# Performance work log

Measured on AMD Instinct MI355X. Metric: run time of the kernel, lower is better.

## Reference

```python
import jax, jax.numpy as jnp
from jax import lax
import numpy as np

B, T, D, H = 64, 512, 1024, 1024


def setup_inputs() -> dict:
    key = jax.random.key(0)
    ks = jax.random.split(key, 4)
    # glorot-ish scaling for stable tanh/sigmoid dynamics
    w_scale = (2.0 / (D + H + 2 * H)) ** 0.5
    u_scale = (2.0 / (D + H + H)) ** 0.5
    return {
        "x": jax.random.normal(ks[0], (B, T, D), dtype=jnp.float32),
        "h0": jax.random.normal(ks[1], (B, H), dtype=jnp.float32),
        "W": jax.random.normal(ks[2], (D + H, 2 * H), dtype=jnp.float32) * w_scale,
        "W_b": jnp.zeros((2 * H,), dtype=jnp.float32),
        "U": jax.random.normal(ks[3], (D + H, H), dtype=jnp.float32) * u_scale,
        "U_b": jnp.zeros((H,), dtype=jnp.float32),
    }


def reference(x, h0, W, W_b, U, U_b):
    """GRUCell from bzhangGo/lrn run over a sequence via lax.scan.

    Per step (faithful to the keras cell):
      gi = sigmoid([x, h] @ W + W_b)   # [B, 2H]
      r, u = gi[:, :H], gi[:, H:]
      c = tanh([x, r*h] @ U + U_b)     # [B, H]
      h = u*h + (1-u)*c
    """
    units = W_b.shape[0] // 2

    def step(h, xt):
        gi = jax.nn.sigmoid(jnp.concatenate([xt, h], axis=-1) @ W + W_b)  # [B, 2H]
        r = gi[:, :units]
        u = gi[:, units:]
        c = jnp.tanh(jnp.concatenate([xt, r * h], axis=-1) @ U + U_b)     # [B, H]
        h_new = u * h + (1.0 - u) * c
        return h_new, h_new

    # scan over time: x [B, T, D] -> [T, B, D]
    _, hs = lax.scan(step, h0, jnp.swapaxes(x, 0, 1))
    return jnp.swapaxes(hs, 0, 1)  # [B, T, H]
```

## Files before the change

### kernel.cpp

```cpp
#include <hip/hip_runtime.h>
#include <hip/hip_bf16.h>
#include <stdint.h>


typedef unsigned short u16;
typedef unsigned long long u64;
typedef __attribute__((ext_vector_type(8))) short bf16x8;
typedef __attribute__((ext_vector_type(4))) float f32x4;

constexpr int Bsz = 64, Tt = 512, Dd = 1024, Hh = 1024;
constexpr int Mrows = Bsz * Tt;
constexpr int NP = 3 * Hh;
constexpr int NBLK = 64, THR = 512;

constexpr size_t SZ_XPROJ = (size_t)Mrows * NP * 2;
constexpr size_t SZ_XBF   = (size_t)Mrows * Dd * 2;
constexpr size_t SZ_PT    = (size_t)NP * 1024 * 2;
constexpr size_t SZ_WHT   = (size_t)2048 * 1024 * 2;
constexpr size_t SZ_UHT   = (size_t)1024 * 1024 * 2;
constexpr size_t OFF_XPROJ = 0;
constexpr size_t OFF_XBF   = OFF_XPROJ + SZ_XPROJ;
constexpr size_t OFF_PT    = OFF_XBF + SZ_XBF;
constexpr size_t OFF_WHT   = OFF_PT + SZ_PT;
constexpr size_t OFF_UHT   = OFF_WHT + SZ_WHT;
constexpr size_t OFF_HG    = OFF_UHT + SZ_UHT;
constexpr size_t OFF_RHG   = OFF_HG  + 131072;
constexpr size_t OFF_BAR   = OFF_RHG + 131072;
constexpr size_t WS_NEEDED = OFF_BAR + 4096;

__device__ __forceinline__ float b2f(u16 u) {
  union { unsigned i; float f; } x; x.i = ((unsigned)u) << 16; return x.f;
}
__device__ __forceinline__ u16 f2b(float f) {
  union { float f; unsigned i; } x; x.f = f;
  unsigned r = (x.i >> 16) & 1u;
  return (u16)((x.i + 0x7fffu + r) >> 16);
}
__device__ __forceinline__ float sigmoidf_(float x) { return 1.0f / (1.0f + __expf(-x)); }
__device__ __forceinline__ float tanhf_(float x) { return 1.0f - 2.0f / (__expf(2.0f * x) + 1.0f); }

__device__ __forceinline__ u64 ldA_u64(const u64* p) {
  return __hip_atomic_load(p, __ATOMIC_RELAXED, __HIP_MEMORY_SCOPE_AGENT);
}
__device__ __forceinline__ void stA_u64(u64* p, u64 v) {
  __hip_atomic_store(p, v, __ATOMIC_RELAXED, __HIP_MEMORY_SCOPE_AGENT);
}
__device__ __forceinline__ unsigned ldA_u32(const unsigned* p) {
  return __hip_atomic_load(p, __ATOMIC_RELAXED, __HIP_MEMORY_SCOPE_AGENT);
}
__device__ __forceinline__ void stA_u32(unsigned* p, unsigned v) {
  __hip_atomic_store(p, v, __ATOMIC_RELAXED, __HIP_MEMORY_SCOPE_AGENT);
}

__device__ __forceinline__ void drain_vm() {
  asm volatile("s_waitcnt vmcnt(0)" ::: "memory");
}
__device__ __forceinline__ void bar_lds() {
  asm volatile("s_waitcnt lgkmcnt(0)\n\ts_barrier" ::: "memory");
}
__device__ __forceinline__ void bar_x() {
  asm volatile("s_barrier" ::: "memory");
}
__device__ __forceinline__ void lds_arrive(unsigned* c) {
  __hip_atomic_fetch_add(c, 1u, __ATOMIC_RELAXED, __HIP_MEMORY_SCOPE_WORKGROUP);
}
__device__ __forceinline__ unsigned lds_peek(unsigned* c) {
  return __hip_atomic_load(c, __ATOMIC_RELAXED, __HIP_MEMORY_SCOPE_WORKGROUP);
}

__device__ __forceinline__ void gl2lds16(const void* g, void* l) {
  __builtin_amdgcn_global_load_lds(
      (const __attribute__((address_space(1))) void*)g,
      (__attribute__((address_space(3))) void*)l, 16, 0, 0);
}

__global__ void k_prep_x(const float* __restrict__ x, u16* __restrict__ xbf,
                         const float* __restrict__ h0, u16* __restrict__ h_g,
                         unsigned* __restrict__ bar) {
  size_t i = (size_t)blockIdx.x * blockDim.x + threadIdx.x;
  size_t stride = (size_t)gridDim.x * blockDim.x;
  if (i < 1024) bar[i] = 0u;
  for (size_t k = i; k < (size_t)Mrows * Dd; k += stride) xbf[k] = f2b(x[k]);
  for (size_t k = i; k < (size_t)Bsz * Hh; k += stride) {
    int r = (int)(k & 15), c = (int)((k >> 4) & 1023), g = (int)(k >> 14);
    h_g[k] = f2b(h0[(size_t)(g * 16 + r) * 1024 + c]);
  }
}

__global__ void k_prep_w(const float* __restrict__ W, const float* __restrict__ U,
                         u16* __restrict__ Pt, u16* __restrict__ Wht, u16* __restrict__ Uht) {
  int k = blockIdx.y, xb = blockIdx.x, tid = threadIdx.x;
  if (xb < 12) {
    int n = xb * 256 + tid;
    float v = (n < 2048) ? W[(size_t)k * 2048 + n] : U[(size_t)k * 1024 + (n - 2048)];
    Pt[(size_t)n * 1024 + k] = f2b(v);
  } else if (xb < 20) {
    int n = (xb - 12) * 256 + tid;
    Wht[(size_t)n * 1024 + k] = f2b(W[(size_t)(1024 + k) * 2048 + n]);
  } else {
    int n = (xb - 20) * 256 + tid;
    Uht[(size_t)n * 1024 + k] = f2b(U[(size_t)(1024 + k) * 1024 + n]);
  }
}

__global__ void k_ws_too_small(float* out) {
  out[threadIdx.x] = 12345.0f;
}

__global__ void k_gemm(const u16* __restrict__ xbf, const u16* __restrict__ Pt,
                       const float* __restrict__ Wb, const float* __restrict__ Ub,
                       u16* __restrict__ xproj) {
  __shared__ u16 As[128 * 32];
  __shared__ u16 Bs[128 * 32];
  const int tid = threadIdx.x, lane = tid & 63, w = tid >> 6;
  const int l15 = lane & 15, q = lane >> 4;
  const int bm = blockIdx.x, bn = blockIdx.y;
  const int wm = w >> 1, wn = w & 1;
  const int lr = lane >> 2;
  const int lc = (lane & 3) * 8;
  f32x4 acc[4][4] = {};
  for (int kt = 0; kt < 32; ++kt) {
    __syncthreads();
    {
      const u16* ga = xbf + (size_t)(bm * 128 + w * 32 + lr) * 1024 + kt * 32 + lc;
      gl2lds16(ga, As + w * 1024);
      gl2lds16(ga + 16 * 1024, As + w * 1024 + 512);
      const u16* gb = Pt + (size_t)(bn * 128 + w * 32 + lr) * 1024 + kt * 32 + lc;
      gl2lds16(gb, Bs + w * 1024);
      gl2lds16(gb + 16 * 1024, Bs + w * 1024 + 512);
    }
    __syncthreads();
    bf16x8 af[4], bfr[4];
#pragma unroll
    for (int i = 0; i < 4; ++i)
      af[i] = *(const bf16x8*)(As + (wm * 64 + i * 16 + l15) * 32 + q * 8);
#pragma unroll
    for (int j = 0; j < 4; ++j)
      bfr[j] = *(const bf16x8*)(Bs + (wn * 64 + j * 16 + l15) * 32 + q * 8);
#pragma unroll
    for (int i = 0; i < 4; ++i)
#pragma unroll
      for (int j = 0; j < 4; ++j)
        acc[i][j] = __builtin_amdgcn_mfma_f32_16x16x32_bf16(af[i], bfr[j], acc[i][j], 0, 0, 0);
  }
#pragma unroll
  for (int j = 0; j < 4; ++j) {
    int n = bn * 128 + wn * 64 + j * 16 + l15;
    float bias = (n < 2048) ? Wb[n] : Ub[n - 2048];
#pragma unroll
    for (int i = 0; i < 4; ++i) {
#pragma unroll
      for (int r = 0; r < 4; ++r) {
        int m = bm * 128 + wm * 64 + i * 16 + q * 4 + r;
        xproj[(size_t)m * NP + n] = f2b(acc[i][j][r] + bias);
      }
    }
  }
}

__device__ __forceinline__ void stage_tile(const u64* g64, u16* hs, int tid) {
#pragma unroll
  for (int i = 0; i < 2; ++i) {
    int z = i * THR + tid;
    int rr = z & 3, cq = z >> 2;
    const u64* p = g64 + cq * 16 + rr;
    u64 v0 = ldA_u64(p);
    u64 v1 = ldA_u64(p + 4);
    u64 v2 = ldA_u64(p + 8);
    u64 v3 = ldA_u64(p + 12);
#pragma unroll
    for (int k = 0; k < 4; ++k) {
      int r = rr * 4 + k;
      u64 wv = (u64)(u16)(v0 >> (16 * k))
             | ((u64)(u16)(v1 >> (16 * k)) << 16)
             | ((u64)(u16)(v2 >> (16 * k)) << 32)
             | ((u64)(u16)(v3 >> (16 * k)) << 48);
      *(u64*)(hs + r * 1032 + cq * 4) = wv;
    }
  }
}

__global__ void __launch_bounds__(THR, 2)
k_seq(const u16* __restrict__ xproj, const u16* __restrict__ Wht,
      const u16* __restrict__ Uht, const float* __restrict__ h0,
      u16* __restrict__ h_g, u16* __restrict__ rh_g,
      float* __restrict__ out, unsigned* __restrict__ bar) {
  __shared__ u16 hs[16 * 1032];
  __shared__ f32x4 red[4][64];
  __shared__ unsigned acnt;
  const int tid = threadIdx.x, lane = tid & 63, w = tid >> 6;
  const int l15 = lane & 15, q = lane >> 4;
  const int b = blockIdx.x;
  const int mh = b & 3;
  const int rbase = mh * 16;
  const int bq = b >> 2;
  const int half = w >> 1;
  const int odd = w & 1;
  const int a_nt = odd ? (bq * 4 + half) : (64 + bq * 4 + half);
  const int a_col = a_nt * 16 + l15;
  const int b_col = (bq * 4 + half) * 16 + l15;

  bf16x8 wa[32];
  { const u16* p = Wht + (size_t)a_col * 1024 + q * 8;
#pragma unroll
    for (int s = 0; s < 32; ++s) wa[s] = *(const bf16x8*)(p + s * 32); }
  bf16x8 wb[16];
  { const u16* p = Uht + (size_t)b_col * 1024 + odd * 512 + q * 8;
#pragma unroll
    for (int s = 0; s < 16; ++s) wb[s] = *(const bf16x8*)(p + s * 32); }

  float hp[4];
#pragma unroll
  for (int r = 0; r < 4; ++r) hp[r] = h0[(size_t)(rbase + q * 4 + r) * 1024 + b_col];

  float gxp[4];
#pragma unroll
  for (int r = 0; r < 4; ++r)
    gxp[r] = b2f(xproj[(size_t)((rbase + q * 4 + r) * Tt + 0) * NP + a_col]);
  float uxp[4] = {0.f, 0.f, 0.f, 0.f};
  if (!odd) {
#pragma unroll
    for (int r = 0; r < 4; ++r)
      uxp[r] = b2f(xproj[(size_t)((rbase + q * 4 + r) * Tt + 0) * NP + 2048 + b_col]);
  }

  const u64* hg64 = (const u64*)h_g + mh * 4096;
  const u64* rg64 = (const u64*)rh_g + mh * 4096;
  const int swb = mh + 4 * l15;

  if (tid == 0) acnt = 0;
  __syncthreads();

  unsigned bct = 0;
  unsigned atgt = 0;
#pragma unroll 1
  for (int t = 0; t < Tt; ++t) {
    stage_tile(hg64, hs, tid);
    bar_lds();

    f32x4 acc = {0.f, 0.f, 0.f, 0.f}, acc2 = {0.f, 0.f, 0.f, 0.f};
    {
      const u16* hb = hs + l15 * 1032 + q * 8;
#pragma unroll
      for (int s = 0; s < 32; s += 2) {
        bf16x8 a0 = *(const bf16x8*)(hb + s * 32);
        bf16x8 a1 = *(const bf16x8*)(hb + (s + 1) * 32);
        acc  = __builtin_amdgcn_mfma_f32_16x16x32_bf16(a0, wa[s], acc, 0, 0, 0);
        acc2 = __builtin_amdgcn_mfma_f32_16x16x32_bf16(a1, wa[s + 1], acc2, 0, 0, 0);
      }
      acc += acc2;
    }
    float uvr[4];
    if (odd) {
      u64 pk = 0;
#pragma unroll
      for (int r = 0; r < 4; ++r) {
        int lrow = q * 4 + r;
        float g = sigmoidf_(acc[r] + gxp[r]);
        float hcell = b2f(hs[lrow * 1032 + a_col]);
        pk |= (u64)f2b(g * hcell) << (16 * r);
      }
      stA_u64((u64*)rh_g + mh * 4096 + a_col * 4 + q, pk);
    } else {
#pragma unroll
      for (int r = 0; r < 4; ++r) uvr[r] = sigmoidf_(acc[r] + gxp[r]);
    }
    drain_vm();
    if (lane == 0) lds_arrive(&acnt);
    atgt += 8; ++bct;
    if (w == 0) {
      while (lds_peek(&acnt) < atgt) {}
      if (lane == 0) stA_u32(bar + (b << 4), bct);
      while (__ballot(ldA_u32(bar + (swb << 4)) < bct) != 0ull) {}
    }
    bar_x();

    stage_tile(rg64, hs, tid);
    bar_lds();

    f32x4 accb = {0.f, 0.f, 0.f, 0.f}, accb2 = {0.f, 0.f, 0.f, 0.f};
    {
      const u16* rb = hs + l15 * 1032 + odd * 512 + q * 8;
#pragma unroll
      for (int s = 0; s < 16; s += 2) {
        bf16x8 a0 = *(const bf16x8*)(rb + s * 32);
        bf16x8 a1 = *(const bf16x8*)(rb + (s + 1) * 32);
        accb  = __builtin_amdgcn_mfma_f32_16x16x32_bf16(a0, wb[s], accb, 0, 0, 0);
        accb2 = __builtin_amdgcn_mfma_f32_16x16x32_bf16(a1, wb[s + 1], accb2, 0, 0, 0);
      }
      accb += accb2;
    }
    if (odd) red[half][lane] = accb;
    bar_lds();
    float hn_[4];
    if (!odd) {
      accb += red[half][lane];
      u64 pk = 0;
#pragma unroll
      for (int r = 0; r < 4; ++r) {
        float c = tanhf_(accb[r] + uxp[r]);
        float hn = uvr[r] * hp[r] + (1.0f - uvr[r]) * c;
        hp[r] = hn; hn_[r] = hn;
        pk |= (u64)f2b(hn) << (16 * r);
      }
      stA_u64((u64*)h_g + mh * 4096 + b_col * 4 + q, pk);
    }
    drain_vm();
    if (lane == 0) lds_arrive(&acnt);
    atgt += 8; ++bct;
    if (!odd) {
#pragma unroll
      for (int r = 0; r < 4; ++r)
        out[((size_t)(rbase + q * 4 + r) * Tt + t) * 1024 + b_col] = hn_[r];
    }
    if (t + 1 < Tt) {
#pragma unroll
      for (int r = 0; r < 4; ++r)
        gxp[r] = b2f(xproj[(size_t)((rbase + q * 4 + r) * Tt + (t + 1)) * NP + a_col]);
      if (!odd) {
#pragma unroll
        for (int r = 0; r < 4; ++r)
          uxp[r] = b2f(xproj[(size_t)((rbase + q * 4 + r) * Tt + (t + 1)) * NP + 2048 + b_col]);
      }
      if (w == 0) {
        while (lds_peek(&acnt) < atgt) {}
        if (lane == 0) stA_u32(bar + (b << 4), bct);
        while (__ballot(ldA_u32(bar + (swb << 4)) < bct) != 0ull) {}
      }
      bar_x();
    }
  }
}

extern "C" void kernel_launch(void* const* d_in, const int* in_sizes, int n_in,
                              void* d_out, int out_size, void* d_ws, size_t ws_size,
                              hipStream_t stream) {
  const float* x  = (const float*)d_in[0];
  const float* h0 = (const float*)d_in[1];
  const float* W  = (const float*)d_in[2];
  const float* Wb = (const float*)d_in[3];
  const float* U  = (const float*)d_in[4];
  const float* Ub = (const float*)d_in[5];
  float* out = (float*)d_out;

  if (ws_size < WS_NEEDED) {
    k_ws_too_small<<<1, 256, 0, stream>>>(out);
    return;
  }

  char* ws = (char*)d_ws;
  u16* xproj = (u16*)(ws + OFF_XPROJ);
  u16* xbf   = (u16*)(ws + OFF_XBF);
  u16* Pt    = (u16*)(ws + OFF_PT);
  u16* Wht   = (u16*)(ws + OFF_WHT);
  u16* Uht   = (u16*)(ws + OFF_UHT);
  u16* h_g   = (u16*)(ws + OFF_HG);
  u16* rh_g  = (u16*)(ws + OFF_RHG);
  unsigned* bar = (unsigned*)(ws + OFF_BAR);

  k_prep_x<<<2048, 256, 0, stream>>>(x, xbf, h0, h_g, bar);
  k_prep_w<<<dim3(24, 1024), 256, 0, stream>>>(W, U, Pt, Wht, Uht);
  k_gemm<<<dim3(256, 24), 256, 0, stream>>>(xbf, Pt, Wb, Ub, xproj);
  k_seq<<<NBLK, 512, 0, stream>>>(xproj, Wht, Uht, h0, h_g, rh_g, out, bar);
}
```

Measured before the change: 4.870 ms.

## Replace grid barriers with sentinel-polled per-block mailboxes for recurrent state

```diff
diff --git a/kernel.cpp b/kernel.cpp
--- a/kernel.cpp
+++ b/kernel.cpp
@@ -12,6 +12,7 @@
 constexpr int Mrows = Bsz * Tt;
 constexpr int NP = 3 * Hh;
 constexpr int NBLK = 64, THR = 512;
+constexpr u64 SENTV = ~0ull;
 
 constexpr size_t SZ_XPROJ = (size_t)Mrows * NP * 2;
 constexpr size_t SZ_XBF   = (size_t)Mrows * Dd * 2;
@@ -23,10 +24,10 @@
 constexpr size_t OFF_PT    = OFF_XBF + SZ_XBF;
 constexpr size_t OFF_WHT   = OFF_PT + SZ_PT;
 constexpr size_t OFF_UHT   = OFF_WHT + SZ_WHT;
-constexpr size_t OFF_HG    = OFF_UHT + SZ_UHT;
-constexpr size_t OFF_RHG   = OFF_HG  + 131072;
-constexpr size_t OFF_BAR   = OFF_RHG + 131072;
+constexpr size_t OFF_BAR   = OFF_UHT + SZ_UHT;
 constexpr size_t WS_NEEDED = OFF_BAR + 4096;
+constexpr size_t OFF_HPV = OFF_XBF;
+constexpr size_t OFF_RPV = OFF_XBF + 4194304;
 
 __device__ __forceinline__ float b2f(u16 u) {
   union { unsigned i; float f; } x; x.i = ((unsigned)u) << 16; return x.f;
@@ -61,12 +62,6 @@
 __device__ __forceinline__ void bar_x() {
   asm volatile("s_barrier" ::: "memory");
 }
-__device__ __forceinline__ void lds_arrive(unsigned* c) {
-  __hip_atomic_fetch_add(c, 1u, __ATOMIC_RELAXED, __HIP_MEMORY_SCOPE_WORKGROUP);
-}
-__device__ __forceinline__ unsigned lds_peek(unsigned* c) {
-  return __hip_atomic_load(c, __ATOMIC_RELAXED, __HIP_MEMORY_SCOPE_WORKGROUP);
-}
 
 __device__ __forceinline__ void gl2lds16(const void* g, void* l) {
   __builtin_amdgcn_global_load_lds(
@@ -75,16 +70,11 @@
 }
 
 __global__ void k_prep_x(const float* __restrict__ x, u16* __restrict__ xbf,
-                         const float* __restrict__ h0, u16* __restrict__ h_g,
                          unsigned* __restrict__ bar) {
   size_t i = (size_t)blockIdx.x * blockDim.x + threadIdx.x;
   size_t stride = (size_t)gridDim.x * blockDim.x;
   if (i < 1024) bar[i] = 0u;
   for (size_t k = i; k < (size_t)Mrows * Dd; k += stride) xbf[k] = f2b(x[k]);
-  for (size_t k = i; k < (size_t)Bsz * Hh; k += stride) {
-    int r = (int)(k & 15), c = (int)((k >> 4) & 1023), g = (int)(k >> 14);
-    h_g[k] = f2b(h0[(size_t)(g * 16 + r) * 1024 + c]);
-  }
 }
 
 __global__ void k_prep_w(const float* __restrict__ W, const float* __restrict__ U,
@@ -158,36 +148,48 @@
   }
 }
 
-__device__ __forceinline__ void stage_tile(const u64* g64, u16* hs, int tid) {
-#pragma unroll
-  for (int i = 0; i < 2; ++i) {
-    int z = i * THR + tid;
-    int rr = z & 3, cq = z >> 2;
-    const u64* p = g64 + cq * 16 + rr;
-    u64 v0 = ldA_u64(p);
-    u64 v1 = ldA_u64(p + 4);
-    u64 v2 = ldA_u64(p + 8);
-    u64 v3 = ldA_u64(p + 12);
+__device__ __forceinline__ void stage_poll(u64* g, u16* hs, int tid) {
+  u64 vv0[4], vv1[4];
+  const int z0 = tid, z1 = THR + tid;
+  const int rr0 = z0 & 3, cq0 = z0 >> 2;
+  const int rr1 = z1 & 3, cq1 = z1 >> 2;
+  u64* p0 = g + cq0 * 16 + rr0;
+  u64* p1 = g + cq1 * 16 + rr1;
+  vv0[0] = ldA_u64(p0); vv0[1] = ldA_u64(p0 + 4);
+  vv0[2] = ldA_u64(p0 + 8); vv0[3] = ldA_u64(p0 + 12);
+  vv1[0] = ldA_u64(p1); vv1[1] = ldA_u64(p1 + 4);
+  vv1[2] = ldA_u64(p1 + 8); vv1[3] = ldA_u64(p1 + 12);
+  for (;;) {
+    bool any = false;
 #pragma unroll
     for (int k = 0; k < 4; ++k) {
-      int r = rr * 4 + k;
-      u64 wv = (u64)(u16)(v0 >> (16 * k))
-             | ((u64)(u16)(v1 >> (16 * k)) << 16)
-             | ((u64)(u16)(v2 >> (16 * k)) << 32)
-             | ((u64)(u16)(v3 >> (16 * k)) << 48);
-      *(u64*)(hs + r * 1032 + cq * 4) = wv;
-    }
-  }
-}
-
-__global__ void __launch_bounds__(THR, 2)
+      if (vv0[k] == SENTV) { vv0[k] = ldA_u64(p0 + 4 * k); if (vv0[k] == SENTV) any = true; }
+      if (vv1[k] == SENTV) { vv1[k] = ldA_u64(p1 + 4 * k); if (vv1[k] == SENTV) any = true; }
+    }
+    if (!any) break;
+  }
+#pragma unroll
+  for (int k = 0; k < 4; ++k) {
+    int r0 = rr0 * 4 + k;
+    u64 w0 = (u64)(u16)(vv0[0] >> (16 * k)) | ((u64)(u16)(vv0[1] >> (16 * k)) << 16)
+           | ((u64)(u16)(vv0[2] >> (16 * k)) << 32) | ((u64)(u16)(vv0[3] >> (16 * k)) << 48);
+    *(u64*)(hs + r0 * 1032 + cq0 * 4) = w0;
+    int r1 = rr1 * 4 + k;
+    u64 w1 = (u64)(u16)(vv1[0] >> (16 * k)) | ((u64)(u16)(vv1[1] >> (16 * k)) << 16)
+           | ((u64)(u16)(vv1[2] >> (16 * k)) << 32) | ((u64)(u16)(vv1[3] >> (16 * k)) << 48);
+    *(u64*)(hs + r1 * 1032 + cq1 * 4) = w1;
+  }
+  stA_u64(p0, SENTV); stA_u64(p0 + 4, SENTV); stA_u64(p0 + 8, SENTV); stA_u64(p0 + 12, SENTV);
+  stA_u64(p1, SENTV); stA_u64(p1 + 4, SENTV); stA_u64(p1 + 8, SENTV); stA_u64(p1 + 12, SENTV);
+}
+
+__global__ void __launch_bounds__(THR, 1)
 k_seq(const u16* __restrict__ xproj, const u16* __restrict__ Wht,
       const u16* __restrict__ Uht, const float* __restrict__ h0,
-      u16* __restrict__ h_g, u16* __restrict__ rh_g,
+      u64* __restrict__ h_pv, u64* __restrict__ rh_pv,
       float* __restrict__ out, unsigned* __restrict__ bar) {
   __shared__ u16 hs[16 * 1032];
   __shared__ f32x4 red[4][64];
-  __shared__ unsigned acnt;
   const int tid = threadIdx.x, lane = tid & 63, w = tid >> 6;
   const int l15 = lane & 15, q = lane >> 4;
   const int b = blockIdx.x;
@@ -224,18 +226,28 @@
       uxp[r] = b2f(xproj[(size_t)((rbase + q * 4 + r) * Tt + 0) * NP + 2048 + b_col]);
   }
 
-  const u64* hg64 = (const u64*)h_g + mh * 4096;
-  const u64* rg64 = (const u64*)rh_g + mh * 4096;
-  const int swb = mh + 4 * l15;
-
-  if (tid == 0) acnt = 0;
+  u64* myh = h_pv + (size_t)b * 8192;
+  u64* myr = rh_pv + (size_t)b * 8192;
+  for (int z = tid; z < 4096; z += THR) {
+    int col = z >> 2, qq = z & 3;
+    u64 v = 0;
+#pragma unroll
+    for (int k = 0; k < 4; ++k)
+      v |= (u64)f2b(h0[(size_t)(rbase + qq * 4 + k) * 1024 + col]) << (16 * k);
+    stA_u64(myh + z, v);
+    stA_u64(myh + 4096 + z, SENTV);
+    stA_u64(myr + z, SENTV);
+    stA_u64(myr + 4096 + z, SENTV);
+  }
   __syncthreads();
-
-  unsigned bct = 0;
-  unsigned atgt = 0;
+  if (tid == 0) stA_u32(bar + (b << 4), 1u);
+  if (tid < 64) { while (ldA_u32(bar + (tid << 4)) < 1u) {} }
+  __syncthreads();
+
 #pragma unroll 1
   for (int t = 0; t < Tt; ++t) {
-    stage_tile(hg64, hs, tid);
+    const int p = t & 1;
+    stage_poll(myh + p * 4096, hs, tid);
     bar_lds();
 
     f32x4 acc = {0.f, 0.f, 0.f, 0.f}, acc2 = {0.f, 0.f, 0.f, 0.f};
@@ -260,22 +272,18 @@
         float hcell = b2f(hs[lrow * 1032 + a_col]);
         pk |= (u64)f2b(g * hcell) << (16 * r);
       }
-      stA_u64((u64*)rh_g + mh * 4096 + a_col * 4 + q, pk);
+      drain_vm();
+      const size_t slot = (size_t)p * 4096 + a_col * 4 + q;
+#pragma unroll
+      for (int j = 0; j < 16; ++j)
+        stA_u64(rh_pv + (size_t)(4 * j + mh) * 8192 + slot, pk);
     } else {
 #pragma unroll
       for (int r = 0; r < 4; ++r) uvr[r] = sigmoidf_(acc[r] + gxp[r]);
     }
-    drain_vm();
-    if (lane == 0) lds_arrive(&acnt);
-    atgt += 8; ++bct;
-    if (w == 0) {
-      while (lds_peek(&acnt) < atgt) {}
-      if (lane == 0) stA_u32(bar + (b << 4), bct);
-      while (__ballot(ldA_u32(bar + (swb << 4)) < bct) != 0ull) {}
-    }
     bar_x();
 
-    stage_tile(rg64, hs, tid);
+    stage_poll(myr + p * 4096, hs, tid);
     bar_lds();
 
     f32x4 accb = {0.f, 0.f, 0.f, 0.f}, accb2 = {0.f, 0.f, 0.f, 0.f};
@@ -292,9 +300,9 @@
     }
     if (odd) red[half][lane] = accb;
     bar_lds();
-    float hn_[4];
     if (!odd) {
       accb += red[half][lane];
+      float hn_[4];
       u64 pk = 0;
 #pragma unroll
       for (int r = 0; r < 4; ++r) {
@@ -303,12 +311,11 @@
         hp[r] = hn; hn_[r] = hn;
         pk |= (u64)f2b(hn) << (16 * r);
       }
-      stA_u64((u64*)h_g + mh * 4096 + b_col * 4 + q, pk);
-    }
-    drain_vm();
-    if (lane == 0) lds_arrive(&acnt);
-    atgt += 8; ++bct;
-    if (!odd) {
+      drain_vm();
+      const size_t slot = (size_t)((t + 1) & 1) * 4096 + b_col * 4 + q;
+#pragma unroll
+      for (int j = 0; j < 16; ++j)
+        stA_u64(h_pv + (size_t)(4 * j + mh) * 8192 + slot, pk);
 #pragma unroll
       for (int r = 0; r < 4; ++r)
         out[((size_t)(rbase + q * 4 + r) * Tt + t) * 1024 + b_col] = hn_[r];
@@ -322,12 +329,6 @@
         for (int r = 0; r < 4; ++r)
           uxp[r] = b2f(xproj[(size_t)((rbase + q * 4 + r) * Tt + (t + 1)) * NP + 2048 + b_col]);
       }
-      if (w == 0) {
-        while (lds_peek(&acnt) < atgt) {}
-        if (lane == 0) stA_u32(bar + (b << 4), bct);
-        while (__ballot(ldA_u32(bar + (swb << 4)) < bct) != 0ull) {}
-      }
-      bar_x();
     }
   }
 }
@@ -354,12 +355,12 @@
   u16* Pt    = (u16*)(ws + OFF_PT);
   u16* Wht   = (u16*)(ws + OFF_WHT);
   u16* Uht   = (u16*)(ws + OFF_UHT);
-  u16* h_g   = (u16*)(ws + OFF_HG);
-  u16* rh_g  = (u16*)(ws + OFF_RHG);
+  u64* h_pv  = (u64*)(ws + OFF_HPV);
+  u64* rh_pv = (u64*)(ws + OFF_RPV);
   unsigned* bar = (unsigned*)(ws + OFF_BAR);
 
-  k_prep_x<<<2048, 256, 0, stream>>>(x, xbf, h0, h_g, bar);
+  k_prep_x<<<2048, 256, 0, stream>>>(x, xbf, bar);
   k_prep_w<<<dim3(24, 1024), 256, 0, stream>>>(W, U, Pt, Wht, Uht);
   k_gemm<<<dim3(256, 24), 256, 0, stream>>>(xbf, Pt, Wb, Ub, xproj);
-  k_seq<<<NBLK, 512, 0, stream>>>(xproj, Wht, Uht, h0, h_g, rh_g, out, bar);
-}
+  k_seq<<<NBLK, 512, 0, stream>>>(xproj, Wht, Uht, h0, h_pv, rh_pv, out, bar);
+}
```

Measured after the change: 6.808 ms. +39.8%, slower.
